# Kernel optimization log

Hardware: AMD Instinct MI355X
Metric: run time of the kernel (lower is better)

The kernel has to match this reference:

```python
import jax, jax.numpy as jnp
import numpy as np

D_MODEL = 512
N_HEADS = 8
D_K = 64
B, T = 64, 256


def setup_inputs() -> dict:
    key = jax.random.key(0)
    ks = jax.random.split(key, 5)
    x = jax.random.normal(ks[0], (B, T, D_MODEL), dtype=jnp.float32)
    s = 1.0 / np.sqrt(D_MODEL)
    Wq = jax.random.normal(ks[1], (N_HEADS, D_MODEL, D_K), dtype=jnp.float32) * s
    Wk = jax.random.normal(ks[2], (N_HEADS, D_MODEL, D_K), dtype=jnp.float32) * s
    Wv = jax.random.normal(ks[3], (N_HEADS, D_MODEL, D_K), dtype=jnp.float32) * s
    Wo = jax.random.normal(ks[4], (N_HEADS * D_K, D_MODEL), dtype=jnp.float32) * s
    return {"x": x, "Wq": Wq, "Wk": Wk, "Wv": Wv, "Wo": Wo}


def reference(x, Wq, Wk, Wv, Wo):
    Bc, Tc, C = x.shape  # C == d_model; source scales by C**0.5, not sqrt(d_k)
    q = jnp.einsum('btc,hcd->bhtd', x, Wq)
    k = jnp.einsum('btc,hcd->bhtd', x, Wk)
    v = jnp.einsum('btc,hcd->bhtd', x, Wv)
    scores = jnp.einsum('bhtd,bhsd->bhts', q, k) / jnp.sqrt(jnp.float32(C))
    causal = jnp.tril(jnp.ones((Tc, Tc), dtype=bool))
    scores = jnp.where(causal, scores, -jnp.inf)
    attn = jax.nn.softmax(scores, axis=-1)  # dropout = identity in eval mode
    out = jnp.einsum('bhts,bhsd->bhtd', attn, v)
    out = out.transpose(0, 2, 1, 3).reshape(Bc, Tc, -1)  # concat heads
    return out @ Wo  # final dropout = identity in eval mode
```

## Files before the change

### kernel.cpp

```cpp
#include <hip/hip_runtime.h>
#include <hip/hip_bf16.h>

typedef __attribute__((ext_vector_type(4))) float f32x4;
typedef __attribute__((ext_vector_type(8))) short bf16x8;
typedef __attribute__((ext_vector_type(4))) short s16x4;
typedef __attribute__((ext_vector_type(4))) unsigned int u32x4;

#define DEV static __device__ __forceinline__

DEV unsigned short f2b(float f) {
  union { float f; unsigned int u; } v; v.f = f;
  unsigned int u = v.u;
  return (unsigned short)((u + 0x7fffu + ((u >> 16) & 1u)) >> 16);
}

DEV void gll16(const void* g, void* l) {
  __builtin_amdgcn_global_load_lds((__attribute__((address_space(1))) void*)g,
                                   (__attribute__((address_space(3))) void*)l,
                                   16, 0, 0);
}

__global__ __launch_bounds__(256) void prep(const float* __restrict__ x,
                                            const float* __restrict__ Wq,
                                            const float* __restrict__ Wk,
                                            const float* __restrict__ Wv,
                                            const float* __restrict__ Wo,
                                            unsigned short* __restrict__ xb,
                                            unsigned short* __restrict__ Wt,
                                            unsigned short* __restrict__ WoT) {
  const int bid = blockIdx.x;
  if (bid < 8192) {
    int id = bid * 256 + threadIdx.x;
    f32x4 v = *(const f32x4*)(x + (long)id * 4);
    s16x4 o;
    o.x = (short)f2b(v.x); o.y = (short)f2b(v.y);
    o.z = (short)f2b(v.z); o.w = (short)f2b(v.w);
    *(s16x4*)(xb + (long)id * 4) = o;
    return;
  }

  __shared__ unsigned int L[64 * 65];
  const int tx = threadIdx.x & 63;
  const int ty = threadIdx.x >> 6;

  int tb = bid - 8192;
  if (tb < 192) {
    int proj = tb >> 6, h = (tb >> 3) & 7, c0 = (tb & 7) << 6;
    const float* W = (proj == 0) ? Wq : ((proj == 1) ? Wk : Wv);
    const float* base = W + (long)h * 32768 + (long)c0 * 64;
#pragma unroll
    for (int i = 0; i < 16; i++) {
      int c = ty + i * 4;
      L[tx * 65 + c] = f2b(base[(long)c * 64 + tx]);
    }
    __syncthreads();
    unsigned short* out = Wt + ((long)(proj * 512 + h * 64)) * 512 + c0;
#pragma unroll
    for (int i = 0; i < 16; i++) {
      int d = ty + i * 4;
      out[(long)d * 512 + tx] = (unsigned short)L[d * 65 + tx];
    }
  } else {
    int t = tb - 192;
    int n0 = (t >> 3) << 6, c0 = (t & 7) << 6;
#pragma unroll
    for (int i = 0; i < 16; i++) {
      int c = ty + i * 4;
      L[tx * 65 + c] = f2b(Wo[(long)(c0 + c) * 512 + n0 + tx]);
    }
    __syncthreads();
    unsigned short* out = WoT + (long)n0 * 512 + c0;
#pragma unroll
    for (int i = 0; i < 16; i++) {
      int n = ty + i * 4;
      out[(long)n * 512 + tx] = (unsigned short)L[n * 65 + tx];
    }
  }
}

template <int F32OUT>
__global__ __launch_bounds__(256, 2) void gemm_bt(const unsigned short* __restrict__ A,
                                                  const unsigned short* __restrict__ BT,
                                                  void* __restrict__ Cv,
                                                  int N) {
  const int K = 512;
  __shared__ unsigned short As[2][128 * 64];
  __shared__ unsigned short Bs[2][128 * 64];

  const int tid = threadIdx.x;
  const int wave = tid >> 6, lane = tid & 63;
  const int quad = lane >> 4, l16 = lane & 15;
  const int wm = wave >> 1, wn = wave & 1;

  const int NB = N >> 7;
  const int nwg = gridDim.x;
  const int q = nwg >> 3, r = nwg & 7;
  const int xcd = blockIdx.x & 7, ci = blockIdx.x >> 3;
  const int wg = (xcd < r ? xcd * (q + 1) : r * (q + 1) + (xcd - r) * q) + ci;
  const int bn = wg % NB;
  const int bm = wg / NB;

  const int srow = lane >> 3;
  const int scol = ((lane & 7) ^ srow) * 8;

  f32x4 acc[4][4] = {};

  auto stage = [&](int kk, int buf) {
#pragma unroll
    for (int s = 0; s < 4; s++) {
      int seg = wave * 4 + s;
      int row = seg * 8 + srow;
      gll16(A + (long)(bm * 128 + row) * K + kk + scol, &As[buf][seg * 512]);
      gll16(BT + (long)(bn * 128 + row) * K + kk + scol, &Bs[buf][seg * 512]);
    }
  };

  auto compute = [&](int buf) {
#pragma unroll
    for (int kc = 0; kc < 2; kc++) {
      const int rq = (((kc * 4 + quad) ^ (l16 & 7)) * 8);
      bf16x8 af[4], bfv[4];
#pragma unroll
      for (int mt = 0; mt < 4; mt++)
        af[mt] = *(const bf16x8*)(&As[buf][(wm * 64 + mt * 16 + l16) * 64 + rq]);
#pragma unroll
      for (int nt = 0; nt < 4; nt++)
        bfv[nt] = *(const bf16x8*)(&Bs[buf][(wn * 64 + nt * 16 + l16) * 64 + rq]);
#pragma unroll
      for (int mt = 0; mt < 4; mt++)
#pragma unroll
        for (int nt = 0; nt < 4; nt++)
          acc[mt][nt] = __builtin_amdgcn_mfma_f32_16x16x32_bf16(af[mt], bfv[nt], acc[mt][nt], 0, 0, 0);
    }
  };

  stage(0, 0);
  asm volatile("s_waitcnt vmcnt(0)" ::: "memory");
  __builtin_amdgcn_s_barrier();
  __builtin_amdgcn_sched_barrier(0);

  int cur = 0;
#pragma unroll
  for (int t = 0; t < 8; t++) {
    if (t < 7) stage((t + 1) * 64, cur ^ 1);
    __builtin_amdgcn_sched_barrier(0);
    compute(cur);
    if (t < 7) {
      asm volatile("s_waitcnt vmcnt(0)" ::: "memory");
      __builtin_amdgcn_s_barrier();
      __builtin_amdgcn_sched_barrier(0);
      cur ^= 1;
    }
  }

#pragma unroll
  for (int mt = 0; mt < 4; mt++) {
#pragma unroll
    for (int nt = 0; nt < 4; nt++) {
      int row0 = bm * 128 + wm * 64 + mt * 16 + quad * 4;
      int col = bn * 128 + wn * 64 + nt * 16 + l16;
      if (F32OUT) {
        float* cp = (float*)Cv + (long)row0 * N + col;
#pragma unroll
        for (int r2 = 0; r2 < 4; r2++)
          cp[(long)r2 * N] = acc[mt][nt][r2];
      } else {
        unsigned short* cp = (unsigned short*)Cv + (long)row0 * N + col;
#pragma unroll
        for (int r2 = 0; r2 < 4; r2++)
          cp[(long)r2 * N] = f2b(acc[mt][nt][r2]);
      }
    }
  }
}

__global__ __launch_bounds__(256, 2) void attn(const unsigned short* __restrict__ QKV,
                                               unsigned short* __restrict__ AO) {
  const int bh = blockIdx.x;
  const int b = bh >> 3, h = bh & 7;
  const int tid = threadIdx.x;
  const int wave = tid >> 6, lane = tid & 63;
  const int quad = lane >> 4, l16 = lane & 15;

  __shared__ unsigned short Kl[256 * 64];
  __shared__ unsigned short Vt[64 * 264];
  __shared__ unsigned short Pl[4][32 * 40];

  const unsigned short* Qb = QKV + (long)b * 256 * 1536 + h * 64;
  const unsigned short* Kb = Qb + 512;
  const unsigned short* Vb = Qb + 1024;

  {
    int r = lane >> 3, cg = lane & 7;
#pragma unroll
    for (int s = 0; s < 8; s++) {
      int seg = wave * 8 + s;
      gll16(Kb + (long)(seg * 8 + r) * 1536 + ((cg ^ r) * 8), Kl + seg * 512);
    }
  }
  {
    int j = tid;
    const unsigned short* vp = Vb + (long)j * 1536;
#pragma unroll
    for (int g = 0; g < 8; g++) {
      union { u32x4 v; unsigned short s[8]; } d;
      d.v = *(const u32x4*)(vp + g * 8);
#pragma unroll
      for (int q = 0; q < 8; q++)
        Vt[(g * 8 + q) * 264 + j] = d.s[q];
    }
  }
  const int tiles[2] = {wave, 7 - wave};
  bf16x8 qf[2][2][2];
#pragma unroll
  for (int ti = 0; ti < 2; ti++)
#pragma unroll
    for (int kc = 0; kc < 2; kc++)
#pragma unroll
      for (int mt = 0; mt < 2; mt++)
        qf[ti][kc][mt] = *(const bf16x8*)(Qb +
            (long)(tiles[ti] * 32 + mt * 16 + l16) * 1536 + kc * 32 + quad * 8);

  __syncthreads();

  f32x4 O[2][2][4] = {};
  float lsum[2][2][4] = {};
  const float scale = 0.044194173824159216f;

#pragma unroll
  for (int ti = 0; ti < 2; ti++) {
    const int t = tiles[ti];
    for (int c32 = 0; c32 <= t; c32++) {
      f32x4 S[2][2] = {};
#pragma unroll
      for (int kc = 0; kc < 2; kc++) {
        bf16x8 kbf[2];
#pragma unroll
        for (int st = 0; st < 2; st++) {
          int jrow = c32 * 32 + st * 16 + l16;
          kbf[st] = *(const bf16x8*)(Kl + jrow * 64 + (((kc * 4 + quad) ^ (jrow & 7)) * 8));
        }
#pragma unroll
        for (int mt = 0; mt < 2; mt++)
#pragma unroll
          for (int st = 0; st < 2; st++)
            S[mt][st] = __builtin_amdgcn_mfma_f32_16x16x32_bf16(qf[ti][kc][mt], kbf[st], S[mt][st], 0, 0, 0);
      }
      const bool diag = (c32 == t);
#pragma unroll
      for (int mt = 0; mt < 2; mt++)
#pragma unroll
        for (int st = 0; st < 2; st++)
#pragma unroll
          for (int r = 0; r < 4; r++) {
            int trow = mt * 16 + quad * 4 + r;
            float p = __expf(S[mt][st][r] * scale);
            if (diag && (st * 16 + l16 > trow)) p = 0.0f;
            lsum[ti][mt][r] += p;
            Pl[wave][trow * 40 + st * 16 + l16] = f2b(p);
          }
      bf16x8 pa[2], vbf[4];
#pragma unroll
      for (int mt = 0; mt < 2; mt++)
        pa[mt] = *(const bf16x8*)(&Pl[wave][(mt * 16 + l16) * 40 + quad * 8]);
#pragma unroll
      for (int dt = 0; dt < 4; dt++)
        vbf[dt] = *(const bf16x8*)(Vt + (dt * 16 + l16) * 264 + c32 * 32 + quad * 8);
#pragma unroll
      for (int mt = 0; mt < 2; mt++)
#pragma unroll
        for (int dt = 0; dt < 4; dt++)
          O[ti][mt][dt] = __builtin_amdgcn_mfma_f32_16x16x32_bf16(pa[mt], vbf[dt], O[ti][mt][dt], 0, 0, 0);
    }
  }

  float linv[2][2][4];
#pragma unroll
  for (int ti = 0; ti < 2; ti++)
#pragma unroll
    for (int mt = 0; mt < 2; mt++)
#pragma unroll
      for (int r = 0; r < 4; r++) {
        float s = lsum[ti][mt][r];
        s += __shfl_xor(s, 1); s += __shfl_xor(s, 2);
        s += __shfl_xor(s, 4); s += __shfl_xor(s, 8);
        linv[ti][mt][r] = 1.0f / s;
      }
#pragma unroll
  for (int ti = 0; ti < 2; ti++)
#pragma unroll
    for (int mt = 0; mt < 2; mt++)
#pragma unroll
      for (int dt = 0; dt < 4; dt++)
#pragma unroll
        for (int r = 0; r < 4; r++) {
          int t_ = tiles[ti] * 32 + mt * 16 + quad * 4 + r;
          int d = dt * 16 + l16;
          AO[(long)(b * 256 + t_) * 512 + h * 64 + d] = f2b(O[ti][mt][dt][r] * linv[ti][mt][r]);
        }
}

extern "C" void kernel_launch(void* const* d_in, const int* in_sizes, int n_in,
                              void* d_out, int out_size, void* d_ws, size_t ws_size,
                              hipStream_t stream) {
  const float* x  = (const float*)d_in[0];
  const float* Wq = (const float*)d_in[1];
  const float* Wk = (const float*)d_in[2];
  const float* Wv = (const float*)d_in[3];
  const float* Wo = (const float*)d_in[4];

  unsigned short* Wt  = (unsigned short*)d_ws;
  unsigned short* WoT = Wt + 1536 * 512;
  unsigned short* xb  = WoT + 512 * 512;
  unsigned short* QKV = xb + (long)16384 * 512;
  unsigned short* AO  = QKV + (long)16384 * 1536;
  float* out = (float*)d_out;

  prep<<<8448, 256, 0, stream>>>(x, Wq, Wk, Wv, Wo, xb, Wt, WoT);

  gemm_bt<0><<<1536, 256, 0, stream>>>(xb, Wt, (void*)QKV, 1536);

  attn<<<512, 256, 0, stream>>>(QKV, AO);

  gemm_bt<1><<<512, 256, 0, stream>>>(AO, WoT, (void*)out, 512);
}
```

Measured before the change: 156.3 us.

## Fuse QKV projection into attention kernel, keeping Q/K/V in shared memory

Replaces the separate QKV GEMM and attention kernels with one 512-thread kernel per (batch, head). Each block computes its 256x192 Q/K/V slice from x and the weights, writes it straight into swizzled LDS (V transposed), then runs causal attention. The attention key-chunks are split across wave pairs, whose partial outputs and row sums are combined through LDS. This removes the QKV global round trip and one launch. In exchange it uses large LDS, recomputes x tile loads per head, and has an odd 8x3 accumulator tiling.

```diff
diff --git a/kernel.cpp b/kernel.cpp
--- a/kernel.cpp
+++ b/kernel.cpp
@@ -78,40 +78,43 @@
   }
 }
 
-template <int F32OUT>
-__global__ __launch_bounds__(256, 2) void gemm_bt(const unsigned short* __restrict__ A,
-                                                  const unsigned short* __restrict__ BT,
-                                                  void* __restrict__ Cv,
-                                                  int N) {
-  const int K = 512;
-  __shared__ unsigned short As[2][128 * 64];
-  __shared__ unsigned short Bs[2][128 * 64];
+__global__ __launch_bounds__(512, 2) void qkv_attn(const unsigned short* __restrict__ xb,
+                                                   const unsigned short* __restrict__ Wt,
+                                                   unsigned short* __restrict__ AO) {
+  __shared__ unsigned short SM[59904];
+  const int QS_OFF = 0, KL_OFF = 16384, VT_OFF = 32768, PL_OFF = 49664;
+  const int ASO[2] = {0, 16384};
+  const int BSO[2] = {32768, 45056};
 
   const int tid = threadIdx.x;
   const int wave = tid >> 6, lane = tid & 63;
   const int quad = lane >> 4, l16 = lane & 15;
-  const int wm = wave >> 1, wn = wave & 1;
-
-  const int NB = N >> 7;
-  const int nwg = gridDim.x;
-  const int q = nwg >> 3, r = nwg & 7;
+
   const int xcd = blockIdx.x & 7, ci = blockIdx.x >> 3;
-  const int wg = (xcd < r ? xcd * (q + 1) : r * (q + 1) + (xcd - r) * q) + ci;
-  const int bn = wg % NB;
-  const int bm = wg / NB;
-
+  const int wg = xcd * 64 + ci;
+  const int b = wg >> 3, h = wg & 7;
+
+  const unsigned short* Ag = xb + (long)b * 256 * 512;
+
+  const int wm = wave >> 2, wn = wave & 3;
   const int srow = lane >> 3;
   const int scol = ((lane & 7) ^ srow) * 8;
 
-  f32x4 acc[4][4] = {};
+  f32x4 acc[8][3] = {};
 
   auto stage = [&](int kk, int buf) {
 #pragma unroll
     for (int s = 0; s < 4; s++) {
       int seg = wave * 4 + s;
       int row = seg * 8 + srow;
-      gll16(A + (long)(bm * 128 + row) * K + kk + scol, &As[buf][seg * 512]);
-      gll16(BT + (long)(bn * 128 + row) * K + kk + scol, &Bs[buf][seg * 512]);
+      gll16(Ag + (long)row * 512 + kk + scol, SM + ASO[buf] + seg * 512);
+    }
+#pragma unroll
+    for (int s = 0; s < 3; s++) {
+      int seg = wave * 3 + s;
+      int proj = seg >> 3;
+      int wrow = proj * 512 + h * 64 + (seg & 7) * 8 + srow;
+      gll16(Wt + (long)wrow * 512 + kk + scol, SM + BSO[buf] + seg * 512);
     }
   };
 
@@ -119,17 +122,17 @@
 #pragma unroll
     for (int kc = 0; kc < 2; kc++) {
       const int rq = (((kc * 4 + quad) ^ (l16 & 7)) * 8);
-      bf16x8 af[4], bfv[4];
-#pragma unroll
-      for (int mt = 0; mt < 4; mt++)
-        af[mt] = *(const bf16x8*)(&As[buf][(wm * 64 + mt * 16 + l16) * 64 + rq]);
-#pragma unroll
-      for (int nt = 0; nt < 4; nt++)
-        bfv[nt] = *(const bf16x8*)(&Bs[buf][(wn * 64 + nt * 16 + l16) * 64 + rq]);
-#pragma unroll
-      for (int mt = 0; mt < 4; mt++)
-#pragma unroll
-        for (int nt = 0; nt < 4; nt++)
+      bf16x8 af[8], bfv[3];
+#pragma unroll
+      for (int mt = 0; mt < 8; mt++)
+        af[mt] = *(const bf16x8*)(SM + ASO[buf] + (wm * 128 + mt * 16 + l16) * 64 + rq);
+#pragma unroll
+      for (int nt = 0; nt < 3; nt++)
+        bfv[nt] = *(const bf16x8*)(SM + BSO[buf] + (wn * 48 + nt * 16 + l16) * 64 + rq);
+#pragma unroll
+      for (int mt = 0; mt < 8; mt++)
+#pragma unroll
+        for (int nt = 0; nt < 3; nt++)
           acc[mt][nt] = __builtin_amdgcn_mfma_f32_16x16x32_bf16(af[mt], bfv[nt], acc[mt][nt], 0, 0, 0);
     }
   };
@@ -153,6 +156,242 @@
     }
   }
 
+  __syncthreads();
+#pragma unroll
+  for (int mt = 0; mt < 8; mt++) {
+#pragma unroll
+    for (int nt = 0; nt < 3; nt++) {
+      const int g = wn * 48 + nt * 16;
+      const int proj = g >> 6;
+      const int j0 = wm * 128 + mt * 16 + quad * 4;
+      if (proj == 2) {
+        int dcol = (g & 63) + l16;
+        unsigned int w0 = (unsigned)f2b(acc[mt][nt][0]) | ((unsigned)f2b(acc[mt][nt][1]) << 16);
+        unsigned int w1 = (unsigned)f2b(acc[mt][nt][2]) | ((unsigned)f2b(acc[mt][nt][3]) << 16);
+        unsigned int* vp = (unsigned int*)(SM + VT_OFF + dcol * 264 + j0);
+        vp[0] = w0; vp[1] = w1;
+      } else {
+        unsigned short* base = SM + (proj ? KL_OFF : QS_OFF);
+        int d = (g & 63) + l16;
+        int dhi = d >> 3, dlo = d & 7;
+#pragma unroll
+        for (int r2 = 0; r2 < 4; r2++) {
+          int j = j0 + r2;
+          base[j * 64 + ((dhi ^ (j & 7)) * 8) + dlo] = f2b(acc[mt][nt][r2]);
+        }
+      }
+    }
+  }
+  __syncthreads();
+
+  const int u = wave >> 1, par = wave & 1;
+  const int tiles2[2] = {u, 7 - u};
+
+  bf16x8 qf[2][2][2];
+#pragma unroll
+  for (int ti = 0; ti < 2; ti++)
+#pragma unroll
+    for (int kc = 0; kc < 2; kc++)
+#pragma unroll
+      for (int mt = 0; mt < 2; mt++) {
+        int row = tiles2[ti] * 32 + mt * 16 + l16;
+        qf[ti][kc][mt] = *(const bf16x8*)(SM + QS_OFF + row * 64 +
+                                          (((kc * 4 + quad) ^ (row & 7)) * 8));
+      }
+
+  f32x4 O[2][2][4] = {};
+  float lsum[2][2][4] = {};
+  const float scale = 0.044194173824159216f;
+
+#pragma unroll
+  for (int ti = 0; ti < 2; ti++) {
+    const int t = tiles2[ti];
+    for (int c32 = par; c32 <= t; c32 += 2) {
+      f32x4 S[2][2] = {};
+#pragma unroll
+      for (int kc = 0; kc < 2; kc++) {
+        bf16x8 kbf[2];
+#pragma unroll
+        for (int st = 0; st < 2; st++) {
+          int jrow = c32 * 32 + st * 16 + l16;
+          kbf[st] = *(const bf16x8*)(SM + KL_OFF + jrow * 64 +
+                                     (((kc * 4 + quad) ^ (jrow & 7)) * 8));
+        }
+#pragma unroll
+        for (int mt = 0; mt < 2; mt++)
+#pragma unroll
+          for (int st = 0; st < 2; st++)
+            S[mt][st] = __builtin_amdgcn_mfma_f32_16x16x32_bf16(qf[ti][kc][mt], kbf[st], S[mt][st], 0, 0, 0);
+      }
+      const bool diag = (c32 == t);
+#pragma unroll
+      for (int mt = 0; mt < 2; mt++)
+#pragma unroll
+        for (int st = 0; st < 2; st++)
+#pragma unroll
+          for (int r = 0; r < 4; r++) {
+            int trow = mt * 16 + quad * 4 + r;
+            float p = __expf(S[mt][st][r] * scale);
+            if (diag && (st * 16 + l16 > trow)) p = 0.0f;
+            lsum[ti][mt][r] += p;
+            SM[PL_OFF + wave * 1280 + trow * 40 + st * 16 + l16] = f2b(p);
+          }
+      bf16x8 pa[2], vbf[4];
+#pragma unroll
+      for (int mt = 0; mt < 2; mt++)
+        pa[mt] = *(const bf16x8*)(SM + PL_OFF + wave * 1280 + (mt * 16 + l16) * 40 + quad * 8);
+#pragma unroll
+      for (int dt = 0; dt < 4; dt++)
+        vbf[dt] = *(const bf16x8*)(SM + VT_OFF + (dt * 16 + l16) * 264 + c32 * 32 + quad * 8);
+#pragma unroll
+      for (int mt = 0; mt < 2; mt++)
+#pragma unroll
+        for (int dt = 0; dt < 4; dt++)
+          O[ti][mt][dt] = __builtin_amdgcn_mfma_f32_16x16x32_bf16(pa[mt], vbf[dt], O[ti][mt][dt], 0, 0, 0);
+    }
+  }
+
+  float lred[2][2][4];
+#pragma unroll
+  for (int ti = 0; ti < 2; ti++)
+#pragma unroll
+    for (int mt = 0; mt < 2; mt++)
+#pragma unroll
+      for (int r = 0; r < 4; r++) {
+        float s = lsum[ti][mt][r];
+        s += __shfl_xor(s, 1); s += __shfl_xor(s, 2);
+        s += __shfl_xor(s, 4); s += __shfl_xor(s, 8);
+        lred[ti][mt][r] = s;
+      }
+
+  __syncthreads();
+
+  float* Oscr = (float*)SM;
+  float* Lscr = (float*)(SM + PL_OFF);
+
+  if (par == 1) {
+#pragma unroll
+    for (int ti = 0; ti < 2; ti++)
+#pragma unroll
+      for (int mt = 0; mt < 2; mt++)
+#pragma unroll
+        for (int dt = 0; dt < 4; dt++)
+#pragma unroll
+          for (int r = 0; r < 4; r++)
+            Oscr[u * 4096 + (ti * 32 + mt * 16 + quad * 4 + r) * 64 + dt * 16 + l16] = O[ti][mt][dt][r];
+    if (l16 == 0)
+#pragma unroll
+      for (int ti = 0; ti < 2; ti++)
+#pragma unroll
+        for (int mt = 0; mt < 2; mt++)
+#pragma unroll
+          for (int r = 0; r < 4; r++)
+            Lscr[u * 64 + ti * 32 + mt * 16 + quad * 4 + r] = lred[ti][mt][r];
+  }
+  __syncthreads();
+
+  if (par == 0) {
+    float linv[2][2][4];
+#pragma unroll
+    for (int ti = 0; ti < 2; ti++)
+#pragma unroll
+      for (int mt = 0; mt < 2; mt++)
+#pragma unroll
+        for (int r = 0; r < 4; r++)
+          linv[ti][mt][r] = 1.0f / (lred[ti][mt][r] +
+                                    Lscr[u * 64 + ti * 32 + mt * 16 + quad * 4 + r]);
+#pragma unroll
+    for (int ti = 0; ti < 2; ti++)
+#pragma unroll
+      for (int mt = 0; mt < 2; mt++)
+#pragma unroll
+        for (int dt = 0; dt < 4; dt++)
+#pragma unroll
+          for (int r = 0; r < 4; r++) {
+            float o = O[ti][mt][dt][r] +
+                      Oscr[u * 4096 + (ti * 32 + mt * 16 + quad * 4 + r) * 64 + dt * 16 + l16];
+            int t_ = tiles2[ti] * 32 + mt * 16 + quad * 4 + r;
+            int d = dt * 16 + l16;
+            AO[(long)(b * 256 + t_) * 512 + h * 64 + d] = f2b(o * linv[ti][mt][r]);
+          }
+  }
+}
+
+template <int F32OUT>
+__global__ __launch_bounds__(256, 2) void gemm_bt(const unsigned short* __restrict__ A,
+                                                  const unsigned short* __restrict__ BT,
+                                                  void* __restrict__ Cv,
+                                                  int N) {
+  const int K = 512;
+  __shared__ unsigned short As[2][128 * 64];
+  __shared__ unsigned short Bs[2][128 * 64];
+
+  const int tid = threadIdx.x;
+  const int wave = tid >> 6, lane = tid & 63;
+  const int quad = lane >> 4, l16 = lane & 15;
+  const int wm = wave >> 1, wn = wave & 1;
+
+  const int NB = N >> 7;
+  const int nwg = gridDim.x;
+  const int q = nwg >> 3, r = nwg & 7;
+  const int xcd = blockIdx.x & 7, ci = blockIdx.x >> 3;
+  const int wg = (xcd < r ? xcd * (q + 1) : r * (q + 1) + (xcd - r) * q) + ci;
+  const int bn = wg % NB;
+  const int bm = wg / NB;
+
+  const int srow = lane >> 3;
+  const int scol = ((lane & 7) ^ srow) * 8;
+
+  f32x4 acc[4][4] = {};
+
+  auto stage = [&](int kk, int buf) {
+#pragma unroll
+    for (int s = 0; s < 4; s++) {
+      int seg = wave * 4 + s;
+      int row = seg * 8 + srow;
+      gll16(A + (long)(bm * 128 + row) * K + kk + scol, &As[buf][seg * 512]);
+      gll16(BT + (long)(bn * 128 + row) * K + kk + scol, &Bs[buf][seg * 512]);
+    }
+  };
+
+  auto compute = [&](int buf) {
+#pragma unroll
+    for (int kc = 0; kc < 2; kc++) {
+      const int rq = (((kc * 4 + quad) ^ (l16 & 7)) * 8);
+      bf16x8 af[4], bfv[4];
+#pragma unroll
+      for (int mt = 0; mt < 4; mt++)
+        af[mt] = *(const bf16x8*)(&As[buf][(wm * 64 + mt * 16 + l16) * 64 + rq]);
+#pragma unroll
+      for (int nt = 0; nt < 4; nt++)
+        bfv[nt] = *(const bf16x8*)(&Bs[buf][(wn * 64 + nt * 16 + l16) * 64 + rq]);
+#pragma unroll
+      for (int mt = 0; mt < 4; mt++)
+#pragma unroll
+        for (int nt = 0; nt < 4; nt++)
+          acc[mt][nt] = __builtin_amdgcn_mfma_f32_16x16x32_bf16(af[mt], bfv[nt], acc[mt][nt], 0, 0, 0);
+    }
+  };
+
+  stage(0, 0);
+  asm volatile("s_waitcnt vmcnt(0)" ::: "memory");
+  __builtin_amdgcn_s_barrier();
+  __builtin_amdgcn_sched_barrier(0);
+
+  int cur = 0;
+#pragma unroll
+  for (int t = 0; t < 8; t++) {
+    if (t < 7) stage((t + 1) * 64, cur ^ 1);
+    __builtin_amdgcn_sched_barrier(0);
+    compute(cur);
+    if (t < 7) {
+      asm volatile("s_waitcnt vmcnt(0)" ::: "memory");
+      __builtin_amdgcn_s_barrier();
+      __builtin_amdgcn_sched_barrier(0);
+      cur ^= 1;
+    }
+  }
+
 #pragma unroll
   for (int mt = 0; mt < 4; mt++) {
 #pragma unroll
@@ -172,132 +411,6 @@
       }
     }
   }
-}
-
-__global__ __launch_bounds__(256, 2) void attn(const unsigned short* __restrict__ QKV,
-                                               unsigned short* __restrict__ AO) {
-  const int bh = blockIdx.x;
-  const int b = bh >> 3, h = bh & 7;
-  const int tid = threadIdx.x;
-  const int wave = tid >> 6, lane = tid & 63;
-  const int quad = lane >> 4, l16 = lane & 15;
-
-  __shared__ unsigned short Kl[256 * 64];
-  __shared__ unsigned short Vt[64 * 264];
-  __shared__ unsigned short Pl[4][32 * 40];
-
-  const unsigned short* Qb = QKV + (long)b * 256 * 1536 + h * 64;
-  const unsigned short* Kb = Qb + 512;
-  const unsigned short* Vb = Qb + 1024;
-
-  {
-    int r = lane >> 3, cg = lane & 7;
-#pragma unroll
-    for (int s = 0; s < 8; s++) {
-      int seg = wave * 8 + s;
-      gll16(Kb + (long)(seg * 8 + r) * 1536 + ((cg ^ r) * 8), Kl + seg * 512);
-    }
-  }
-  {
-    int j = tid;
-    const unsigned short* vp = Vb + (long)j * 1536;
-#pragma unroll
-    for (int g = 0; g < 8; g++) {
-      union { u32x4 v; unsigned short s[8]; } d;
-      d.v = *(const u32x4*)(vp + g * 8);
-#pragma unroll
-      for (int q = 0; q < 8; q++)
-        Vt[(g * 8 + q) * 264 + j] = d.s[q];
-    }
-  }
-  const int tiles[2] = {wave, 7 - wave};
-  bf16x8 qf[2][2][2];
-#pragma unroll
-  for (int ti = 0; ti < 2; ti++)
-#pragma unroll
-    for (int kc = 0; kc < 2; kc++)
-#pragma unroll
-      for (int mt = 0; mt < 2; mt++)
-        qf[ti][kc][mt] = *(const bf16x8*)(Qb +
-            (long)(tiles[ti] * 32 + mt * 16 + l16) * 1536 + kc * 32 + quad * 8);
-
-  __syncthreads();
-
-  f32x4 O[2][2][4] = {};
-  float lsum[2][2][4] = {};
-  const float scale = 0.044194173824159216f;
-
-#pragma unroll
-  for (int ti = 0; ti < 2; ti++) {
-    const int t = tiles[ti];
-    for (int c32 = 0; c32 <= t; c32++) {
-      f32x4 S[2][2] = {};
-#pragma unroll
-      for (int kc = 0; kc < 2; kc++) {
-        bf16x8 kbf[2];
-#pragma unroll
-        for (int st = 0; st < 2; st++) {
-          int jrow = c32 * 32 + st * 16 + l16;
-          kbf[st] = *(const bf16x8*)(Kl + jrow * 64 + (((kc * 4 + quad) ^ (jrow & 7)) * 8));
-        }
-#pragma unroll
-        for (int mt = 0; mt < 2; mt++)
-#pragma unroll
-          for (int st = 0; st < 2; st++)
-            S[mt][st] = __builtin_amdgcn_mfma_f32_16x16x32_bf16(qf[ti][kc][mt], kbf[st], S[mt][st], 0, 0, 0);
-      }
-      const bool diag = (c32 == t);
-#pragma unroll
-      for (int mt = 0; mt < 2; mt++)
-#pragma unroll
-        for (int st = 0; st < 2; st++)
-#pragma unroll
-          for (int r = 0; r < 4; r++) {
-            int trow = mt * 16 + quad * 4 + r;
-            float p = __expf(S[mt][st][r] * scale);
-            if (diag && (st * 16 + l16 > trow)) p = 0.0f;
-            lsum[ti][mt][r] += p;
-            Pl[wave][trow * 40 + st * 16 + l16] = f2b(p);
-          }
-      bf16x8 pa[2], vbf[4];
-#pragma unroll
-      for (int mt = 0; mt < 2; mt++)
-        pa[mt] = *(const bf16x8*)(&Pl[wave][(mt * 16 + l16) * 40 + quad * 8]);
-#pragma unroll
-      for (int dt = 0; dt < 4; dt++)
-        vbf[dt] = *(const bf16x8*)(Vt + (dt * 16 + l16) * 264 + c32 * 32 + quad * 8);
-#pragma unroll
-      for (int mt = 0; mt < 2; mt++)
-#pragma unroll
-        for (int dt = 0; dt < 4; dt++)
-          O[ti][mt][dt] = __builtin_amdgcn_mfma_f32_16x16x32_bf16(pa[mt], vbf[dt], O[ti][mt][dt], 0, 0, 0);
-    }
-  }
-
-  float linv[2][2][4];
-#pragma unroll
-  for (int ti = 0; ti < 2; ti++)
-#pragma unroll
-    for (int mt = 0; mt < 2; mt++)
-#pragma unroll
-      for (int r = 0; r < 4; r++) {
-        float s = lsum[ti][mt][r];
-        s += __shfl_xor(s, 1); s += __shfl_xor(s, 2);
-        s += __shfl_xor(s, 4); s += __shfl_xor(s, 8);
-        linv[ti][mt][r] = 1.0f / s;
-      }
-#pragma unroll
-  for (int ti = 0; ti < 2; ti++)
-#pragma unroll
-    for (int mt = 0; mt < 2; mt++)
-#pragma unroll
-      for (int dt = 0; dt < 4; dt++)
-#pragma unroll
-        for (int r = 0; r < 4; r++) {
-          int t_ = tiles[ti] * 32 + mt * 16 + quad * 4 + r;
-          int d = dt * 16 + l16;
-          AO[(long)(b * 256 + t_) * 512 + h * 64 + d] = f2b(O[ti][mt][dt][r] * linv[ti][mt][r]);
-        }
 }
 
 extern "C" void kernel_launch(void* const* d_in, const int* in_sizes, int n_in,
@@ -312,15 +425,12 @@
   unsigned short* Wt  = (unsigned short*)d_ws;
   unsigned short* WoT = Wt + 1536 * 512;
   unsigned short* xb  = WoT + 512 * 512;
-  unsigned short* QKV = xb + (long)16384 * 512;
-  unsigned short* AO  = QKV + (long)16384 * 1536;
+  unsigned short* AO  = xb + (long)16384 * 512;
   float* out = (float*)d_out;
 
   prep<<<8448, 256, 0, stream>>>(x, Wq, Wk, Wv, Wo, xb, Wt, WoT);
 
-  gemm_bt<0><<<1536, 256, 0, stream>>>(xb, Wt, (void*)QKV, 1536);
-
-  attn<<<512, 256, 0, stream>>>(QKV, AO);
+  qkv_attn<<<512, 512, 0, stream>>>(xb, Wt, AO);
 
   gemm_bt<1><<<512, 256, 0, stream>>>(AO, WoT, (void*)out, 512);
 }
```

Measured after the change: 148.2 us. -5.1%, faster.
